# Kernel tuning notes

Hardware: AMD Instinct MI355X
Metric: run time of the kernel (lower is better)

The kernel has to match this reference:

```python
import jax, jax.numpy as jnp
import numpy as np

ALPHA = jnp.full((8,), 0.25, dtype=jnp.float32)  # per-class focal alpha
GAMMA = 2.0
TEMP = 0.07
CIRC_TARGET = 1.0
CIRC_WEIGHT = 0.1
MIN_AGREE = 0.6
W_FOCAL, W_CONTRAST, W_CONSENSUS = 1.0, 0.5, 0.3


def setup_inputs() -> dict:
    key = jax.random.key(0)
    k1, k2, k3, k4, k5 = jax.random.split(key, 5)
    return {
        "logits": jax.random.normal(k1, (32, 8, 256, 256), dtype=jnp.float32),
        "target": jax.random.randint(k2, (32, 256, 256), 0, 8, dtype=jnp.int32),
        "features": jax.random.normal(k3, (1024, 512), dtype=jnp.float32),
        "masks": jax.random.uniform(k4, (32, 3, 256, 256), dtype=jnp.float32),
        "method_preds": jax.random.uniform(k5, (3, 32, 256, 256), dtype=jnp.float32),
    }


def focal_loss(logits, target):
    B, C, H, W = logits.shape
    x = logits.transpose(0, 2, 3, 1).reshape(-1, C)  # [BHW, C]
    t = target.reshape(-1)
    logp = jax.nn.log_softmax(x, axis=-1)
    ce = -jnp.take_along_axis(logp, t[:, None], axis=1)[:, 0]
    p = jnp.exp(-ce)
    focal_w = ALPHA[t] * (1.0 - p) ** GAMMA
    return jnp.mean(focal_w * ce)


def contrastive_loss(features):
    Bf = features.shape[0]
    f = features / jnp.linalg.norm(features, axis=1, keepdims=True)
    sim = (f @ f.T) / TEMP  # [Bf, Bf]
    # default labels = arange(Bf//2) tiled twice -> each sample has exactly one
    # positive: its paired view at index (i + Bf//2) % Bf
    pos_idx = (jnp.arange(Bf) + Bf // 2) % Bf
    pos = sim[jnp.arange(Bf), pos_idx]
    diag = jnp.eye(Bf, dtype=bool)
    # logits row i = {positive_i} U negatives_i = all j != i (single positive case)
    masked = jnp.where(diag, -1e30, sim)
    lse = jax.nn.logsumexp(masked, axis=1)
    return jnp.mean(lse - pos)  # CE with target = the (only) positive


def circularity_loss(masks):
    m = masks[:, 0]  # [B, H, W] core channel
    B = m.shape[0]
    area = jnp.sum(m, axis=(1, 2))
    ex = jnp.sum(jnp.abs(m[:, 1:, :] - m[:, :-1, :]), axis=(1, 2))
    ey = jnp.sum(jnp.abs(m[:, :, 1:] - m[:, :, :-1]), axis=(1, 2))
    per = ex + ey
    circ = 4.0 * np.pi * area / jnp.maximum(per, 1e-12) ** 2
    li = jnp.where((area > 0) & (per > 0), (circ - CIRC_TARGET) ** 2, 0.0)
    return CIRC_WEIGHT * jnp.sum(li) / B


def consensus_loss(method_preds):
    K = method_preds.shape[0]
    total, n = 0.0, 0
    for i in range(K):  # K=3 methods -> 3 pairs (fixed, small)
        for j in range(i + 1, K):
            pi, pj = method_preds[i], method_preds[j]
            inter = jnp.sum(pi * pj)
            union = jnp.sum(pi + pj - pi * pj)
            iou = inter / (union + 1e-6)
            total = total + jax.nn.relu(MIN_AGREE - iou)
            n += 1
    return total / n


def reference(logits, target, features, masks, method_preds):
    return (W_FOCAL * focal_loss(logits, target)
            + W_CONTRAST * contrastive_loss(features)
            + circularity_loss(masks)
            + W_CONSENSUS * consensus_loss(method_preds))
```

## Files before the change

kernel.cpp:

```cpp
#include <hip/hip_runtime.h>
#include <math.h>

#define WS_FOCALP 0
#define WS_CONSP  2048
#define WS_AREAP  14336
#define WS_EXP_   14848
#define WS_EYP_   15360
#define WS_POS    15872
#define WS_PART   16896
#define WS_HI_B   393216
#define WS_LO_B   1441792

typedef __attribute__((ext_vector_type(8))) short bf16x8;
typedef __attribute__((ext_vector_type(4))) float f32x4;

__device__ inline float wave_reduce(float v) {
#pragma unroll
  for (int m = 32; m >= 1; m >>= 1) v += __shfl_xor(v, m);
  return v;
}

__device__ inline unsigned short bf16_rne(float x) {
  union { float f; unsigned u; } v; v.f = x;
  unsigned r = v.u + 0x7FFF + ((v.u >> 16) & 1);
  return (unsigned short)(r >> 16);
}
__device__ inline float bf16_f(unsigned short h) {
  union { unsigned u; float f; } v; v.u = ((unsigned)h) << 16; return v.f;
}

__device__ inline float focal_px(float v0, float v1, float v2, float v3,
                                 float v4, float v5, float v6, float v7, int tt) {
  float mx = fmaxf(fmaxf(fmaxf(v0, v1), fmaxf(v2, v3)),
                   fmaxf(fmaxf(v4, v5), fmaxf(v6, v7)));
  float se = __expf(v0 - mx) + __expf(v1 - mx) + __expf(v2 - mx) + __expf(v3 - mx) +
             __expf(v4 - mx) + __expf(v5 - mx) + __expf(v6 - mx) + __expf(v7 - mx);
  float xt = v0;
  xt = (tt == 1) ? v1 : xt;
  xt = (tt == 2) ? v2 : xt;
  xt = (tt == 3) ? v3 : xt;
  xt = (tt == 4) ? v4 : xt;
  xt = (tt == 5) ? v5 : xt;
  xt = (tt == 6) ? v6 : xt;
  xt = (tt == 7) ? v7 : xt;
  float lp = (xt - mx) - __logf(se);
  float p = __expf(lp);
  float om = 1.0f - p;
  return 0.25f * om * om * (-lp);
}

__global__ __launch_bounds__(256) void prep_kernel(const float* __restrict__ feat,
                                                   float* __restrict__ ws) {
  const int tid = threadIdx.x;
  const int lane = tid & 63;
  const int wid = tid >> 6;
  int row = blockIdx.x * 4 + wid;
  const float4* f4 = (const float4*)feat;
  float4 u = f4[row * 128 + lane];
  float4 w = f4[row * 128 + 64 + lane];
  float s = u.x * u.x + u.y * u.y + u.z * u.z + u.w * u.w +
            w.x * w.x + w.y * w.y + w.z * w.z + w.w * w.w;
  s = wave_reduce(s);
  float scale = 3.7796447300922719f / sqrtf(s);
  float g[8] = {u.x * scale, u.y * scale, u.z * scale, u.w * scale,
                w.x * scale, w.y * scale, w.z * scale, w.w * scale};
  unsigned short h[8];
  unsigned short l[8];
#pragma unroll
  for (int i = 0; i < 8; i++) {
    h[i] = bf16_rne(g[i]);
    l[i] = bf16_rne(g[i] - bf16_f(h[i]));
  }
  const int rg = row >> 4, r15 = row & 15;
  int k0 = lane * 4;
  int k1 = 256 + lane * 4;
  int off0 = (rg * 16 + (k0 >> 5)) * 1024 + (((k0 >> 3) & 3) * 16 + r15) * 16 + (k0 & 7) * 2;
  int off1 = (rg * 16 + (k1 >> 5)) * 1024 + (((k1 >> 3) & 3) * 16 + r15) * 16 + (k1 & 7) * 2;
  char* hb = (char*)ws + WS_HI_B;
  char* lb = (char*)ws + WS_LO_B;
  *(ushort4*)(hb + off0) = make_ushort4(h[0], h[1], h[2], h[3]);
  *(ushort4*)(hb + off1) = make_ushort4(h[4], h[5], h[6], h[7]);
  *(ushort4*)(lb + off0) = make_ushort4(l[0], l[1], l[2], l[3]);
  *(ushort4*)(lb + off1) = make_ushort4(l[4], l[5], l[6], l[7]);
}

__global__ __launch_bounds__(256) void fused_kernel(
    const float* __restrict__ logits, const int* __restrict__ target,
    const float* __restrict__ masks, const float* __restrict__ preds,
    float* __restrict__ ws) {
  __shared__ float red[32];
  const int bid = blockIdx.x;
  const int tid = threadIdx.x;
  const int lane = tid & 63;
  const int wid = tid >> 6;

  if (bid < 512) {
    const int rt = bid >> 4;
    const int ct = bid & 15;
    const int wr = wid >> 1, wc = wid & 1;
    const int l15 = lane & 15;
    const int hi8 = lane >> 4;
    const char* HI = (const char*)ws + WS_HI_B;
    const char* LO = (const char*)ws + WS_LO_B;
    const int rga = rt * 2 + wr;
    const int rgb = ct * 4 + wc * 2;
    const int lb16 = lane * 16;

    f32x4 acc0 = {0.f, 0.f, 0.f, 0.f};
    f32x4 acc1 = {0.f, 0.f, 0.f, 0.f};

#pragma unroll 2
    for (int kb = 0; kb < 16; kb++) {
      const char* pA = HI + (rga * 16 + kb) * 1024 + lb16;
      const char* qA = LO + (rga * 16 + kb) * 1024 + lb16;
      const char* pB0 = HI + (rgb * 16 + kb) * 1024 + lb16;
      const char* qB0 = LO + (rgb * 16 + kb) * 1024 + lb16;
      const char* pB1 = HI + ((rgb + 1) * 16 + kb) * 1024 + lb16;
      const char* qB1 = LO + ((rgb + 1) * 16 + kb) * 1024 + lb16;
      bf16x8 ah = *(const bf16x8*)pA;
      bf16x8 al = *(const bf16x8*)qA;
      bf16x8 bh0 = *(const bf16x8*)pB0;
      bf16x8 bl0 = *(const bf16x8*)qB0;
      bf16x8 bh1 = *(const bf16x8*)pB1;
      bf16x8 bl1 = *(const bf16x8*)qB1;
      acc0 = __builtin_amdgcn_mfma_f32_16x16x32_bf16(ah, bh0, acc0, 0, 0, 0);
      acc1 = __builtin_amdgcn_mfma_f32_16x16x32_bf16(ah, bh1, acc1, 0, 0, 0);
      acc0 = __builtin_amdgcn_mfma_f32_16x16x32_bf16(ah, bl0, acc0, 0, 0, 0);
      acc1 = __builtin_amdgcn_mfma_f32_16x16x32_bf16(ah, bl1, acc1, 0, 0, 0);
      acc0 = __builtin_amdgcn_mfma_f32_16x16x32_bf16(al, bh0, acc0, 0, 0, 0);
      acc1 = __builtin_amdgcn_mfma_f32_16x16x32_bf16(al, bh1, acc1, 0, 0, 0);
    }

    float2* part = (float2*)(ws + WS_PART);
    int c0 = ct * 64 + wc * 32 + l15;
    int c1 = c0 + 16;
#pragma unroll
    for (int q = 0; q < 4; q++) {
      int row = rt * 32 + wr * 16 + hi8 * 4 + q;
      int pc = (row + 512) & 1023;
      float v0 = acc0[q], v1 = acc1[q];
      if (c0 == pc) ws[WS_POS + row] = v0;
      if (c1 == pc) ws[WS_POS + row] = v1;
      if (c0 == row) v0 = -1e30f;
      if (c1 == row) v1 = -1e30f;
      float m = fmaxf(v0, v1);
      float s = __expf(v0 - m) + __expf(v1 - m);
#pragma unroll
      for (int d = 1; d < 16; d <<= 1) {
        float mo = __shfl_xor(m, d), so = __shfl_xor(s, d);
        float nm = fmaxf(m, mo);
        s = s * __expf(m - nm) + so * __expf(mo - nm);
        m = nm;
      }
      if (l15 == 0) part[row * 32 + ct * 2 + wc] = make_float2(m, s);
    }
    return;
  }

  const int bid2 = bid - 512;

  if (bid2 < 2048) {
    int t = bid2 * 256 + tid;
    int p4 = t * 4;
    int b = p4 >> 16;
    int hw = p4 & 65535;
    const float* lb = logits + (b << 19) + hw;
    float4 x0 = *(const float4*)(lb + (0 << 16));
    float4 x1 = *(const float4*)(lb + (1 << 16));
    float4 x2 = *(const float4*)(lb + (2 << 16));
    float4 x3 = *(const float4*)(lb + (3 << 16));
    float4 x4 = *(const float4*)(lb + (4 << 16));
    float4 x5 = *(const float4*)(lb + (5 << 16));
    float4 x6 = *(const float4*)(lb + (6 << 16));
    float4 x7 = *(const float4*)(lb + (7 << 16));
    int4 tg = *(const int4*)(target + p4);
    float acc = 0.0f;
    acc += focal_px(x0.x, x1.x, x2.x, x3.x, x4.x, x5.x, x6.x, x7.x, tg.x);
    acc += focal_px(x0.y, x1.y, x2.y, x3.y, x4.y, x5.y, x6.y, x7.y, tg.y);
    acc += focal_px(x0.z, x1.z, x2.z, x3.z, x4.z, x5.z, x6.z, x7.z, tg.z);
    acc += focal_px(x0.w, x1.w, x2.w, x3.w, x4.w, x5.w, x6.w, x7.w, tg.w);
    float v = wave_reduce(acc);
    if (lane == 0) red[wid] = v;
    __syncthreads();
    if (tid == 0) ws[WS_FOCALP + bid2] = red[0] + red[1] + red[2] + red[3];

  } else if (bid2 < 2560) {
    int bi = bid2 - 2048;
    int img = bi >> 4;
    int part = bi & 15;
    const float* mS = masks + img * 3 * 65536;
    const float4* m4 = (const float4*)mS;
    float a = 0.0f, ex = 0.0f, ey = 0.0f;
#pragma unroll
    for (int i = 0; i < 4; i++) {
      int v = tid + 256 * i;
      int rl = v >> 6;
      int c4 = v & 63;
      int row = part * 16 + rl;
      float4 val = m4[row * 64 + c4];
      a += val.x + val.y + val.z + val.w;
      ey += fabsf(val.y - val.x) + fabsf(val.z - val.y) + fabsf(val.w - val.z);
      if (c4 > 0) ey += fabsf(val.x - mS[row * 256 + c4 * 4 - 1]);
      if (row > 0) {
        float4 u = m4[(row - 1) * 64 + c4];
        ex += fabsf(val.x - u.x) + fabsf(val.y - u.y) +
              fabsf(val.z - u.z) + fabsf(val.w - u.w);
      }
    }
    float ra = wave_reduce(a);
    float rx = wave_reduce(ex);
    float ry = wave_reduce(ey);
    if (lane == 0) {
      red[wid + 0] = ra; red[wid + 4] = rx; red[wid + 8] = ry;
    }
    __syncthreads();
    if (tid == 0) {
      ws[WS_AREAP + bi] = red[0] + red[1] + red[2] + red[3];
      ws[WS_EXP_ + bi] = red[4] + red[5] + red[6] + red[7];
      ws[WS_EYP_ + bi] = red[8] + red[9] + red[10] + red[11];
    }

  } else {
    int b = bid2 - 2560;
    int t = b * 256 + tid;
    const float4* q = (const float4*)preds;
    float4 a0 = q[t];
    float4 a1 = q[t + 524288];
    float4 a2 = q[t + 1048576];
    float s0 = a0.x + a0.y + a0.z + a0.w;
    float s1 = a1.x + a1.y + a1.z + a1.w;
    float s2 = a2.x + a2.y + a2.z + a2.w;
    float p01 = a0.x * a1.x + a0.y * a1.y + a0.z * a1.z + a0.w * a1.w;
    float p02 = a0.x * a2.x + a0.y * a2.y + a0.z * a2.z + a0.w * a2.w;
    float p12 = a1.x * a2.x + a1.y * a2.y + a1.z * a2.z + a1.w * a2.w;
    float r0 = wave_reduce(s0);
    float r1 = wave_reduce(s1);
    float r2 = wave_reduce(s2);
    float r3 = wave_reduce(p01);
    float r4 = wave_reduce(p02);
    float r5 = wave_reduce(p12);
    if (lane == 0) {
      red[wid + 0] = r0; red[wid + 4] = r1; red[wid + 8] = r2;
      red[wid + 12] = r3; red[wid + 16] = r4; red[wid + 20] = r5;
    }
    __syncthreads();
    if (tid == 0) {
#pragma unroll
      for (int k = 0; k < 6; k++)
        ws[WS_CONSP + k * 2048 + b] =
            red[k * 4] + red[k * 4 + 1] + red[k * 4 + 2] + red[k * 4 + 3];
    }
  }
}

__global__ __launch_bounds__(1024) void final_kernel(float* __restrict__ ws,
                                                     float* __restrict__ out) {
  __shared__ float red[16][8];
  __shared__ float li_s[32];
  int r = threadIdx.x;
  int lane = r & 63, wid = r >> 6;

  float v[8];
  const float2* part = (const float2*)(ws + WS_PART);
  float M = -1e30f, S = 0.0f;
#pragma unroll
  for (int ctl = 0; ctl < 32; ctl++) {
    float2 p = part[r * 32 + ctl];
    float nm = fmaxf(M, p.x);
    S = S * __expf(M - nm) + p.y * __expf(p.x - nm);
    M = nm;
  }
  v[0] = (M + __logf(S)) - ws[WS_POS + r];
  v[1] = ws[WS_FOCALP + r] + ws[WS_FOCALP + r + 1024];
#pragma unroll
  for (int k = 0; k < 6; k++) {
    const float* p = ws + WS_CONSP + k * 2048;
    v[2 + k] = p[r] + p[r + 1024];
  }
#pragma unroll
  for (int k = 0; k < 8; k++) {
    v[k] = wave_reduce(v[k]);
    if (lane == 0) red[wid][k] = v[k];
  }

  if (r < 512) {
    float a = ws[WS_AREAP + r];
    float ex = ws[WS_EXP_ + r];
    float ey = ws[WS_EYP_ + r];
#pragma unroll
    for (int d = 1; d < 16; d <<= 1) {
      a += __shfl_xor(a, d);
      ex += __shfl_xor(ex, d);
      ey += __shfl_xor(ey, d);
    }
    if ((r & 15) == 0) {
      float per = ex + ey;
      float dd = fmaxf(per, 1e-12f);
      float c = 12.566370614359172f * a / (dd * dd);
      li_s[r >> 4] = (a > 0.0f && per > 0.0f) ? (c - 1.0f) * (c - 1.0f) : 0.0f;
    }
  }
  __syncthreads();

  if (r == 0) {
    float tot[8];
#pragma unroll
    for (int k = 0; k < 8; k++) {
      float t = 0.0f;
#pragma unroll
      for (int i = 0; i < 16; i++) t += red[i][k];
      tot[k] = t;
    }
    float circ = 0.0f;
#pragma unroll
    for (int i = 0; i < 32; i++) circ += li_s[i];
    circ = 0.1f * circ / 32.0f;

    float contr = tot[0] / 1024.0f;
    float focal = tot[1] / 2097152.0f;

    float S0 = tot[2], S1 = tot[3], S2 = tot[4];
    float P01 = tot[5], P02 = tot[6], P12 = tot[7];
    float co = 0.0f;
    co += fmaxf(0.6f - P01 / (S0 + S1 - P01 + 1e-6f), 0.0f);
    co += fmaxf(0.6f - P02 / (S0 + S2 - P02 + 1e-6f), 0.0f);
    co += fmaxf(0.6f - P12 / (S1 + S2 - P12 + 1e-6f), 0.0f);
    co *= (1.0f / 3.0f);

    out[0] = focal + 0.5f * contr + circ + 0.3f * co;
  }
}

extern "C" void kernel_launch(void* const* d_in, const int* in_sizes, int n_in,
                              void* d_out, int out_size, void* d_ws, size_t ws_size,
                              hipStream_t stream) {
  const float* logits = (const float*)d_in[0];
  const int* target = (const int*)d_in[1];
  const float* feat = (const float*)d_in[2];
  const float* masks = (const float*)d_in[3];
  const float* preds = (const float*)d_in[4];
  float* ws = (float*)d_ws;
  float* out = (float*)d_out;

  prep_kernel<<<256, 256, 0, stream>>>(feat, ws);
  fused_kernel<<<5120, 256, 0, stream>>>(logits, target, masks, preds, ws);
  final_kernel<<<1, 1024, 0, stream>>>(ws, out);
}
```

Before: 47.20 us.

## Fold feature prep into streaming kernel and split similarity GEMM into its own launch

The feature normalization and bf16 hi/lo split moves into the large streaming-reduction kernel as extra trailing blocks, and the MFMA similarity GEMM moves into a separate kernel launched afterwards. The GEMM loop is also fully unrolled with hoisted base pointers. The aim is to shorten the serial chain: the small prep step no longer runs alone before the memory-bound reductions. The cost is that the GEMM blocks no longer overlap with the streaming work and now run as a separate launch after it.

```diff
diff --git a/kernel.cpp b/kernel.cpp
--- a/kernel.cpp
+++ b/kernel.cpp
@@ -49,118 +49,18 @@
   return 0.25f * om * om * (-lp);
 }
 
-__global__ __launch_bounds__(256) void prep_kernel(const float* __restrict__ feat,
-                                                   float* __restrict__ ws) {
-  const int tid = threadIdx.x;
-  const int lane = tid & 63;
-  const int wid = tid >> 6;
-  int row = blockIdx.x * 4 + wid;
-  const float4* f4 = (const float4*)feat;
-  float4 u = f4[row * 128 + lane];
-  float4 w = f4[row * 128 + 64 + lane];
-  float s = u.x * u.x + u.y * u.y + u.z * u.z + u.w * u.w +
-            w.x * w.x + w.y * w.y + w.z * w.z + w.w * w.w;
-  s = wave_reduce(s);
-  float scale = 3.7796447300922719f / sqrtf(s);
-  float g[8] = {u.x * scale, u.y * scale, u.z * scale, u.w * scale,
-                w.x * scale, w.y * scale, w.z * scale, w.w * scale};
-  unsigned short h[8];
-  unsigned short l[8];
-#pragma unroll
-  for (int i = 0; i < 8; i++) {
-    h[i] = bf16_rne(g[i]);
-    l[i] = bf16_rne(g[i] - bf16_f(h[i]));
-  }
-  const int rg = row >> 4, r15 = row & 15;
-  int k0 = lane * 4;
-  int k1 = 256 + lane * 4;
-  int off0 = (rg * 16 + (k0 >> 5)) * 1024 + (((k0 >> 3) & 3) * 16 + r15) * 16 + (k0 & 7) * 2;
-  int off1 = (rg * 16 + (k1 >> 5)) * 1024 + (((k1 >> 3) & 3) * 16 + r15) * 16 + (k1 & 7) * 2;
-  char* hb = (char*)ws + WS_HI_B;
-  char* lb = (char*)ws + WS_LO_B;
-  *(ushort4*)(hb + off0) = make_ushort4(h[0], h[1], h[2], h[3]);
-  *(ushort4*)(hb + off1) = make_ushort4(h[4], h[5], h[6], h[7]);
-  *(ushort4*)(lb + off0) = make_ushort4(l[0], l[1], l[2], l[3]);
-  *(ushort4*)(lb + off1) = make_ushort4(l[4], l[5], l[6], l[7]);
-}
-
-__global__ __launch_bounds__(256) void fused_kernel(
+__global__ __launch_bounds__(256) void mega_kernel(
     const float* __restrict__ logits, const int* __restrict__ target,
-    const float* __restrict__ masks, const float* __restrict__ preds,
-    float* __restrict__ ws) {
+    const float* __restrict__ feat, const float* __restrict__ masks,
+    const float* __restrict__ preds, float* __restrict__ ws) {
   __shared__ float red[32];
   const int bid = blockIdx.x;
   const int tid = threadIdx.x;
   const int lane = tid & 63;
   const int wid = tid >> 6;
 
-  if (bid < 512) {
-    const int rt = bid >> 4;
-    const int ct = bid & 15;
-    const int wr = wid >> 1, wc = wid & 1;
-    const int l15 = lane & 15;
-    const int hi8 = lane >> 4;
-    const char* HI = (const char*)ws + WS_HI_B;
-    const char* LO = (const char*)ws + WS_LO_B;
-    const int rga = rt * 2 + wr;
-    const int rgb = ct * 4 + wc * 2;
-    const int lb16 = lane * 16;
-
-    f32x4 acc0 = {0.f, 0.f, 0.f, 0.f};
-    f32x4 acc1 = {0.f, 0.f, 0.f, 0.f};
-
-#pragma unroll 2
-    for (int kb = 0; kb < 16; kb++) {
-      const char* pA = HI + (rga * 16 + kb) * 1024 + lb16;
-      const char* qA = LO + (rga * 16 + kb) * 1024 + lb16;
-      const char* pB0 = HI + (rgb * 16 + kb) * 1024 + lb16;
-      const char* qB0 = LO + (rgb * 16 + kb) * 1024 + lb16;
-      const char* pB1 = HI + ((rgb + 1) * 16 + kb) * 1024 + lb16;
-      const char* qB1 = LO + ((rgb + 1) * 16 + kb) * 1024 + lb16;
-      bf16x8 ah = *(const bf16x8*)pA;
-      bf16x8 al = *(const bf16x8*)qA;
-      bf16x8 bh0 = *(const bf16x8*)pB0;
-      bf16x8 bl0 = *(const bf16x8*)qB0;
-      bf16x8 bh1 = *(const bf16x8*)pB1;
-      bf16x8 bl1 = *(const bf16x8*)qB1;
-      acc0 = __builtin_amdgcn_mfma_f32_16x16x32_bf16(ah, bh0, acc0, 0, 0, 0);
-      acc1 = __builtin_amdgcn_mfma_f32_16x16x32_bf16(ah, bh1, acc1, 0, 0, 0);
-      acc0 = __builtin_amdgcn_mfma_f32_16x16x32_bf16(ah, bl0, acc0, 0, 0, 0);
-      acc1 = __builtin_amdgcn_mfma_f32_16x16x32_bf16(ah, bl1, acc1, 0, 0, 0);
-      acc0 = __builtin_amdgcn_mfma_f32_16x16x32_bf16(al, bh0, acc0, 0, 0, 0);
-      acc1 = __builtin_amdgcn_mfma_f32_16x16x32_bf16(al, bh1, acc1, 0, 0, 0);
-    }
-
-    float2* part = (float2*)(ws + WS_PART);
-    int c0 = ct * 64 + wc * 32 + l15;
-    int c1 = c0 + 16;
-#pragma unroll
-    for (int q = 0; q < 4; q++) {
-      int row = rt * 32 + wr * 16 + hi8 * 4 + q;
-      int pc = (row + 512) & 1023;
-      float v0 = acc0[q], v1 = acc1[q];
-      if (c0 == pc) ws[WS_POS + row] = v0;
-      if (c1 == pc) ws[WS_POS + row] = v1;
-      if (c0 == row) v0 = -1e30f;
-      if (c1 == row) v1 = -1e30f;
-      float m = fmaxf(v0, v1);
-      float s = __expf(v0 - m) + __expf(v1 - m);
-#pragma unroll
-      for (int d = 1; d < 16; d <<= 1) {
-        float mo = __shfl_xor(m, d), so = __shfl_xor(s, d);
-        float nm = fmaxf(m, mo);
-        s = s * __expf(m - nm) + so * __expf(mo - nm);
-        m = nm;
-      }
-      if (l15 == 0) part[row * 32 + ct * 2 + wc] = make_float2(m, s);
-    }
-    return;
-  }
-
-  const int bid2 = bid - 512;
-
-  if (bid2 < 2048) {
-    int t = bid2 * 256 + tid;
+  if (bid < 2048) {
+    int t = bid * 256 + tid;
     int p4 = t * 4;
     int b = p4 >> 16;
     int hw = p4 & 65535;
@@ -182,10 +82,10 @@
     float v = wave_reduce(acc);
     if (lane == 0) red[wid] = v;
     __syncthreads();
-    if (tid == 0) ws[WS_FOCALP + bid2] = red[0] + red[1] + red[2] + red[3];
-
-  } else if (bid2 < 2560) {
-    int bi = bid2 - 2048;
+    if (tid == 0) ws[WS_FOCALP + bid] = red[0] + red[1] + red[2] + red[3];
+
+  } else if (bid < 2560) {
+    int bi = bid - 2048;
     int img = bi >> 4;
     int part = bi & 15;
     const float* mS = masks + img * 3 * 65536;
@@ -220,8 +120,8 @@
       ws[WS_EYP_ + bi] = red[8] + red[9] + red[10] + red[11];
     }
 
-  } else {
-    int b = bid2 - 2560;
+  } else if (bid < 4608) {
+    int b = bid - 2560;
     int t = b * 256 + tid;
     const float4* q = (const float4*)preds;
     float4 a0 = q[t];
@@ -250,6 +150,100 @@
         ws[WS_CONSP + k * 2048 + b] =
             red[k * 4] + red[k * 4 + 1] + red[k * 4 + 2] + red[k * 4 + 3];
     }
+
+  } else {
+    int row = (bid - 4608) * 4 + wid;
+    const float4* f4 = (const float4*)feat;
+    float4 u = f4[row * 128 + lane];
+    float4 w = f4[row * 128 + 64 + lane];
+    float s = u.x * u.x + u.y * u.y + u.z * u.z + u.w * u.w +
+              w.x * w.x + w.y * w.y + w.z * w.z + w.w * w.w;
+    s = wave_reduce(s);
+    float scale = 3.7796447300922719f / sqrtf(s);
+    float g[8] = {u.x * scale, u.y * scale, u.z * scale, u.w * scale,
+                  w.x * scale, w.y * scale, w.z * scale, w.w * scale};
+    unsigned short h[8];
+    unsigned short l[8];
+#pragma unroll
+    for (int i = 0; i < 8; i++) {
+      h[i] = bf16_rne(g[i]);
+      l[i] = bf16_rne(g[i] - bf16_f(h[i]));
+    }
+    const int rg = row >> 4, r15 = row & 15;
+    int k0 = lane * 4;
+    int k1 = 256 + lane * 4;
+    int off0 = (rg * 16 + (k0 >> 5)) * 1024 + (((k0 >> 3) & 3) * 16 + r15) * 16 + (k0 & 7) * 2;
+    int off1 = (rg * 16 + (k1 >> 5)) * 1024 + (((k1 >> 3) & 3) * 16 + r15) * 16 + (k1 & 7) * 2;
+    char* hb = (char*)ws + WS_HI_B;
+    char* lb = (char*)ws + WS_LO_B;
+    *(ushort4*)(hb + off0) = make_ushort4(h[0], h[1], h[2], h[3]);
+    *(ushort4*)(hb + off1) = make_ushort4(h[4], h[5], h[6], h[7]);
+    *(ushort4*)(lb + off0) = make_ushort4(l[0], l[1], l[2], l[3]);
+    *(ushort4*)(lb + off1) = make_ushort4(l[4], l[5], l[6], l[7]);
+  }
+}
+
+__global__ __launch_bounds__(256) void sim_kernel(float* __restrict__ ws) {
+  const int tid = threadIdx.x;
+  const int lane = tid & 63;
+  const int wid = tid >> 6;
+  const int rt = blockIdx.x >> 4, ct = blockIdx.x & 15;
+  const int wr = wid >> 1, wc = wid & 1;
+  const int l15 = lane & 15;
+  const int hi8 = lane >> 4;
+  const char* HI = (const char*)ws + WS_HI_B;
+  const char* LO = (const char*)ws + WS_LO_B;
+  const int rga = rt * 2 + wr;
+  const int rgb = ct * 4 + wc * 2;
+  const int lb16 = lane * 16;
+  const char* pAh = HI + rga * 16384 + lb16;
+  const char* pAl = LO + rga * 16384 + lb16;
+  const char* pB0h = HI + rgb * 16384 + lb16;
+  const char* pB0l = LO + rgb * 16384 + lb16;
+  const char* pB1h = HI + (rgb + 1) * 16384 + lb16;
+  const char* pB1l = LO + (rgb + 1) * 16384 + lb16;
+
+  f32x4 acc0 = {0.f, 0.f, 0.f, 0.f};
+  f32x4 acc1 = {0.f, 0.f, 0.f, 0.f};
+
+#pragma unroll
+  for (int kb = 0; kb < 16; kb++) {
+    bf16x8 ah = *(const bf16x8*)(pAh + kb * 1024);
+    bf16x8 al = *(const bf16x8*)(pAl + kb * 1024);
+    bf16x8 bh0 = *(const bf16x8*)(pB0h + kb * 1024);
+    bf16x8 bl0 = *(const bf16x8*)(pB0l + kb * 1024);
+    bf16x8 bh1 = *(const bf16x8*)(pB1h + kb * 1024);
+    bf16x8 bl1 = *(const bf16x8*)(pB1l + kb * 1024);
+    acc0 = __builtin_amdgcn_mfma_f32_16x16x32_bf16(ah, bh0, acc0, 0, 0, 0);
+    acc1 = __builtin_amdgcn_mfma_f32_16x16x32_bf16(ah, bh1, acc1, 0, 0, 0);
+    acc0 = __builtin_amdgcn_mfma_f32_16x16x32_bf16(ah, bl0, acc0, 0, 0, 0);
+    acc1 = __builtin_amdgcn_mfma_f32_16x16x32_bf16(ah, bl1, acc1, 0, 0, 0);
+    acc0 = __builtin_amdgcn_mfma_f32_16x16x32_bf16(al, bh0, acc0, 0, 0, 0);
+    acc1 = __builtin_amdgcn_mfma_f32_16x16x32_bf16(al, bh1, acc1, 0, 0, 0);
+  }
+
+  float2* part = (float2*)(ws + WS_PART);
+  int c0 = ct * 64 + wc * 32 + l15;
+  int c1 = c0 + 16;
+#pragma unroll
+  for (int q = 0; q < 4; q++) {
+    int row = rt * 32 + wr * 16 + hi8 * 4 + q;
+    int pc = (row + 512) & 1023;
+    float v0 = acc0[q], v1 = acc1[q];
+    if (c0 == pc) ws[WS_POS + row] = v0;
+    if (c1 == pc) ws[WS_POS + row] = v1;
+    if (c0 == row) v0 = -1e30f;
+    if (c1 == row) v1 = -1e30f;
+    float m = fmaxf(v0, v1);
+    float s = __expf(v0 - m) + __expf(v1 - m);
+#pragma unroll
+    for (int d = 1; d < 16; d <<= 1) {
+      float mo = __shfl_xor(m, d), so = __shfl_xor(s, d);
+      float nm = fmaxf(m, mo);
+      s = s * __expf(m - nm) + so * __expf(mo - nm);
+      m = nm;
+    }
+    if (l15 == 0) part[row * 32 + ct * 2 + wc] = make_float2(m, s);
   }
 }
 
@@ -342,7 +336,7 @@
   float* ws = (float*)d_ws;
   float* out = (float*)d_out;
 
-  prep_kernel<<<256, 256, 0, stream>>>(feat, ws);
-  fused_kernel<<<5120, 256, 0, stream>>>(logits, target, masks, preds, ws);
+  mega_kernel<<<4864, 256, 0, stream>>>(logits, target, feat, masks, preds, ws);
+  sim_kernel<<<512, 256, 0, stream>>>(ws);
   final_kernel<<<1, 1024, 0, stream>>>(ws, out);
 }
```

Result: no change. 47.87 us (+1.4%).
